# Optimization experiments

Measured on AMD Instinct MI355X. Metric: run time of the kernel, lower is better.

Reference implementation:

```python
import jax, jax.numpy as jnp
import numpy as np

THRESHOLD = 0.3
STRENGTH = 0.1
MIN_S = 0.0
MAX_S = 0.5
EPS_COS = 1e-8
EPS_LN = 1e-5

B, T, D = 1024, 64, 256
P = 2048
H = 512


def _layernorm(x, g, b):
    mu = x.mean(-1, keepdims=True)
    var = ((x - mu) ** 2).mean(-1, keepdims=True)
    return (x - mu) * jax.lax.rsqrt(var + EPS_LN) * g + b


def setup_inputs() -> dict:
    key = jax.random.key(0)
    ks = jax.random.split(key, 10)
    s = lambda fan_in: 1.0 / np.sqrt(fan_in)
    return {
        "current_feat": jax.random.normal(ks[0], (B, T, D), jnp.float32),
        "prototype": jax.random.normal(ks[1], (P, T, D), jnp.float32),
        "dd_w1": jax.random.normal(ks[2], (2 * D, H), jnp.float32) * s(2 * D),
        "dd_b1": jnp.zeros((H,), jnp.float32),
        "dd_g1": jnp.ones((H,), jnp.float32),
        "dd_be1": jnp.zeros((H,), jnp.float32),
        "dd_w2": jax.random.normal(ks[3], (H, H // 2), jnp.float32) * s(H),
        "dd_b2": jnp.zeros((H // 2,), jnp.float32),
        "dd_w3": jax.random.normal(ks[4], (H // 2, 1), jnp.float32) * s(H // 2),
        "dd_b3": jnp.zeros((1,), jnp.float32),
        "cal_w1": jax.random.normal(ks[5], (D, H), jnp.float32) * s(D),
        "cal_b1": jnp.zeros((H,), jnp.float32),
        "cal_g1": jnp.ones((H,), jnp.float32),
        "cal_be1": jnp.zeros((H,), jnp.float32),
        "cal_w2": jax.random.normal(ks[6], (H, H), jnp.float32) * s(H),
        "cal_b2": jnp.zeros((H,), jnp.float32),
        "cal_w3": jax.random.normal(ks[7], (H, D), jnp.float32) * s(H),
        "cal_b3": jnp.zeros((D,), jnp.float32),
    }


def reference(current_feat, prototype,
              dd_w1, dd_b1, dd_g1, dd_be1, dd_w2, dd_b2, dd_w3, dd_b3,
              cal_w1, cal_b1, cal_g1, cal_be1, cal_w2, cal_b2, cal_w3, cal_b3):
    # --- drift detection ---
    feat_flat = current_feat.mean(axis=1)          # [B, D]
    proto_centers = prototype.mean(axis=1)         # [P, D]
    fn = jnp.maximum(jnp.linalg.norm(feat_flat, axis=-1), EPS_COS)   # [B]
    pn = jnp.maximum(jnp.linalg.norm(proto_centers, axis=-1), EPS_COS)  # [P]
    sim = jnp.einsum('bd,pd->bp', feat_flat, proto_centers) / (fn[:, None] * pn[None, :])
    drift_score = 1.0 - sim                        # [B, P]
    is_drifted = drift_score.mean(axis=0) > THRESHOLD  # [P] bool

    # --- calibration (batched over all P, then masked scatter) ---
    global_mean = feat_flat.mean(axis=0)           # [D]
    concat = jnp.concatenate(
        [proto_centers, jnp.broadcast_to(global_mean, (proto_centers.shape[0], global_mean.shape[0]))], axis=-1)  # [P, 2D]
    h = jax.nn.relu(_layernorm(concat @ dd_w1 + dd_b1, dd_g1, dd_be1))
    h = jax.nn.relu(h @ dd_w2 + dd_b2)
    drift_conf = jax.nn.sigmoid(h @ dd_w3 + dd_b3)[:, 0]  # [P]

    c = jax.nn.relu(_layernorm(proto_centers @ cal_w1 + cal_b1, cal_g1, cal_be1))
    c = jax.nn.relu(c @ cal_w2 + cal_b2)
    delta = c @ cal_w3 + cal_b3                    # [P, D]

    strength = jnp.clip(STRENGTH * drift_conf, MIN_S, MAX_S)  # [P]
    new_center = proto_centers + strength[:, None] * delta    # [P, D]

    calibrated = jnp.where(is_drifted[:, None, None], new_center[:, None, :], prototype)  # [P, T, D]
    return calibrated, drift_score, is_drifted
```

## Files before the change

### kernel.cpp

```cpp
#include <hip/hip_runtime.h>
#include <hip/hip_bf16.h>
#include <math.h>

#define BB 1024
#define TT 64
#define DD 256
#define PP 2048
#define HH 512

typedef __attribute__((ext_vector_type(8))) short short8;
typedef __attribute__((ext_vector_type(4))) float f32x4;

__device__ __forceinline__ float blk_reduce(float v, float* sm) {
    int tid = threadIdx.x;
    #pragma unroll
    for (int o = 32; o > 0; o >>= 1) v += __shfl_down(v, o, 64);
    if ((tid & 63) == 0) sm[tid >> 6] = v;
    __syncthreads();
    float r = sm[0] + sm[1] + sm[2] + sm[3];
    __syncthreads();
    return r;
}

__global__ void reduce_bt(const float* __restrict__ x, float* __restrict__ cent,
                          __hip_bfloat16* __restrict__ centb, float* __restrict__ nrm) {
    __shared__ float sm[4];
    int r = blockIdx.x, d = threadIdx.x;
    const float* p = x + (size_t)r * TT * DD + d;
    float s = 0.f;
    #pragma unroll
    for (int t = 0; t < TT; ++t) s += p[t * DD];
    float m = s * (1.f / TT);
    cent[(size_t)r * DD + d] = m;
    centb[(size_t)r * DD + d] = __float2bfloat16(m);
    float tot = blk_reduce(m * m, sm);
    if (d == 0) nrm[r] = fmaxf(sqrtf(tot), 1e-8f);
}

__global__ void gmean_k(const float* __restrict__ ff, float* __restrict__ gmean) {
    int d = threadIdx.x;
    int b0 = blockIdx.x * 32;
    float s = 0.f;
    for (int b = b0; b < b0 + 32; ++b) s += ff[(size_t)b * DD + d];
    atomicAdd(&gmean[d], s * (1.f / BB));
}

__global__ void addvec_k(const float* __restrict__ gmean, const float* __restrict__ w1,
                         const float* __restrict__ b1, float* __restrict__ av) {
    int j = (blockIdx.x & 1) * 256 + threadIdx.x;
    int k0 = (blockIdx.x >> 1) * 64;
    float s = 0.f;
    for (int k = k0; k < k0 + 64; ++k) s += gmean[k] * w1[(size_t)(DD + k) * HH + j];
    if (k0 == 0) s += b1[j];
    atomicAdd(&av[j], s);
}

__global__ void cvt_all(const float* __restrict__ dd_w1, const float* __restrict__ dd_w2,
                        const float* __restrict__ cal_w1, const float* __restrict__ cal_w2,
                        const float* __restrict__ cal_w3,
                        __hip_bfloat16* __restrict__ t1, __hip_bfloat16* __restrict__ t2,
                        __hip_bfloat16* __restrict__ t3, __hip_bfloat16* __restrict__ t4,
                        __hip_bfloat16* __restrict__ t5) {
    int b = blockIdx.x, tid = threadIdx.x;
    const float* src; __hip_bfloat16* dst; int K, N, base;
    if (b < 512)       { src = dd_w1;  dst = t1; K = 256; N = 512; base = 0; }
    else if (b < 1024) { src = dd_w2;  dst = t2; K = 512; N = 256; base = 512; }
    else if (b < 1536) { src = cal_w1; dst = t3; K = 256; N = 512; base = 1024; }
    else if (b < 2560) { src = cal_w2; dst = t4; K = 512; N = 512; base = 1536; }
    else               { src = cal_w3; dst = t5; K = 512; N = 256; base = 2560; }
    int idx = (b - base) * 256 + tid;
    int n = idx & (N - 1);
    int k = idx >> ((N == 512) ? 9 : 8);
    dst[(size_t)n * K + k] = __float2bfloat16(src[(size_t)k * N + n]);
}

__global__ void sim_mfma(const __hip_bfloat16* __restrict__ A,
                         const __hip_bfloat16* __restrict__ Bt,
                         const float* __restrict__ fn, const float* __restrict__ pn,
                         float* __restrict__ drift, float* __restrict__ colsum) {
    int wid = ((blockIdx.x << 8) + threadIdx.x) >> 6;
    int lane = threadIdx.x & 63;
    int mw = wid >> 6, nw = wid & 63;
    int m0 = mw << 5, n0 = nw << 5;
    int lr = lane & 15, quad = lane >> 4;
    const __hip_bfloat16* pa0 = A + (size_t)(m0 + lr) * DD + quad * 8;
    const __hip_bfloat16* pa1 = pa0 + 16 * DD;
    const __hip_bfloat16* pb0 = Bt + (size_t)(n0 + lr) * DD + quad * 8;
    const __hip_bfloat16* pb1 = pb0 + 16 * DD;
    f32x4 acc00 = {0,0,0,0}, acc01 = {0,0,0,0}, acc10 = {0,0,0,0}, acc11 = {0,0,0,0};
    #pragma unroll
    for (int k = 0; k < DD; k += 32) {
        short8 a0 = *(const short8*)(pa0 + k);
        short8 a1 = *(const short8*)(pa1 + k);
        short8 b0 = *(const short8*)(pb0 + k);
        short8 b1 = *(const short8*)(pb1 + k);
        acc00 = __builtin_amdgcn_mfma_f32_16x16x32_bf16(a0, b0, acc00, 0, 0, 0);
        acc01 = __builtin_amdgcn_mfma_f32_16x16x32_bf16(a0, b1, acc01, 0, 0, 0);
        acc10 = __builtin_amdgcn_mfma_f32_16x16x32_bf16(a1, b0, acc10, 0, 0, 0);
        acc11 = __builtin_amdgcn_mfma_f32_16x16x32_bf16(a1, b1, acc11, 0, 0, 0);
    }
    int col0 = n0 + lr, col1 = col0 + 16;
    float ip0 = 1.f / pn[col0], ip1 = 1.f / pn[col1];
    float cs0 = 0.f, cs1 = 0.f;
    #pragma unroll
    for (int r = 0; r < 4; ++r) {
        int row0 = m0 + quad * 4 + r;
        int row1 = row0 + 16;
        float if0 = 1.f / fn[row0];
        float if1 = 1.f / fn[row1];
        float d00 = 1.f - acc00[r] * if0 * ip0;
        float d01 = 1.f - acc01[r] * if0 * ip1;
        float d10 = 1.f - acc10[r] * if1 * ip0;
        float d11 = 1.f - acc11[r] * if1 * ip1;
        drift[(size_t)row0 * PP + col0] = d00;
        drift[(size_t)row0 * PP + col1] = d01;
        drift[(size_t)row1 * PP + col0] = d10;
        drift[(size_t)row1 * PP + col1] = d11;
        cs0 += d00 + d10;
        cs1 += d01 + d11;
    }
    cs0 += __shfl_xor(cs0, 16, 64); cs0 += __shfl_xor(cs0, 32, 64);
    cs1 += __shfl_xor(cs1, 16, 64); cs1 += __shfl_xor(cs1, 32, 64);
    if (quad == 0) {
        atomicAdd(&colsum[col0], cs0);
        atomicAdd(&colsum[col1], cs1);
    }
}

template <int K, int OUT_BF16, int RELU>
__global__ void gemm_mfma(const __hip_bfloat16* __restrict__ A,
                          const __hip_bfloat16* __restrict__ Bt,
                          const float* __restrict__ bias,
                          void* __restrict__ Cout, int N) {
    int wid = ((blockIdx.x << 8) + threadIdx.x) >> 6;
    int lane = threadIdx.x & 63;
    int nt = N >> 5;
    int mw = wid / nt, nw = wid - mw * nt;
    int m0 = mw << 5, n0 = nw << 5;
    int lr = lane & 15, quad = lane >> 4;
    const __hip_bfloat16* pa0 = A + (size_t)(m0 + lr) * K + quad * 8;
    const __hip_bfloat16* pa1 = pa0 + 16 * K;
    const __hip_bfloat16* pb0 = Bt + (size_t)(n0 + lr) * K + quad * 8;
    const __hip_bfloat16* pb1 = pb0 + 16 * K;
    f32x4 acc00 = {0,0,0,0}, acc01 = {0,0,0,0}, acc10 = {0,0,0,0}, acc11 = {0,0,0,0};
    #pragma unroll
    for (int k = 0; k < K; k += 32) {
        short8 a0 = *(const short8*)(pa0 + k);
        short8 a1 = *(const short8*)(pa1 + k);
        short8 b0 = *(const short8*)(pb0 + k);
        short8 b1 = *(const short8*)(pb1 + k);
        acc00 = __builtin_amdgcn_mfma_f32_16x16x32_bf16(a0, b0, acc00, 0, 0, 0);
        acc01 = __builtin_amdgcn_mfma_f32_16x16x32_bf16(a0, b1, acc01, 0, 0, 0);
        acc10 = __builtin_amdgcn_mfma_f32_16x16x32_bf16(a1, b0, acc10, 0, 0, 0);
        acc11 = __builtin_amdgcn_mfma_f32_16x16x32_bf16(a1, b1, acc11, 0, 0, 0);
    }
    int col0 = n0 + lr, col1 = col0 + 16;
    float bi0 = bias[col0], bi1 = bias[col1];
    #pragma unroll
    for (int r = 0; r < 4; ++r) {
        int row0 = m0 + quad * 4 + r;
        int row1 = row0 + 16;
        float v00 = acc00[r] + bi0, v01 = acc01[r] + bi1;
        float v10 = acc10[r] + bi0, v11 = acc11[r] + bi1;
        if (RELU) {
            v00 = fmaxf(v00, 0.f); v01 = fmaxf(v01, 0.f);
            v10 = fmaxf(v10, 0.f); v11 = fmaxf(v11, 0.f);
        }
        if (OUT_BF16) {
            __hip_bfloat16* C = (__hip_bfloat16*)Cout;
            C[(size_t)row0 * N + col0] = __float2bfloat16(v00);
            C[(size_t)row0 * N + col1] = __float2bfloat16(v01);
            C[(size_t)row1 * N + col0] = __float2bfloat16(v10);
            C[(size_t)row1 * N + col1] = __float2bfloat16(v11);
        } else {
            float* C = (float*)Cout;
            C[(size_t)row0 * N + col0] = v00;
            C[(size_t)row0 * N + col1] = v01;
            C[(size_t)row1 * N + col0] = v10;
            C[(size_t)row1 * N + col1] = v11;
        }
    }
}

__global__ void ln_relu(const float* __restrict__ X, __hip_bfloat16* __restrict__ Y,
                        const float* __restrict__ g, const float* __restrict__ be) {
    __shared__ float sm[4];
    int r = blockIdx.x, tid = threadIdx.x;
    const float* row = X + (size_t)r * HH;
    float x0 = row[tid], x1 = row[tid + 256];
    float mu = blk_reduce(x0 + x1, sm) * (1.f / HH);
    float d0 = x0 - mu, d1 = x1 - mu;
    float var = blk_reduce(d0 * d0 + d1 * d1, sm) * (1.f / HH);
    float rs = rsqrtf(var + 1e-5f);
    float y0 = fmaxf(d0 * rs * g[tid] + be[tid], 0.f);
    float y1 = fmaxf(d1 * rs * g[tid + 256] + be[tid + 256], 0.f);
    __hip_bfloat16* yrow = Y + (size_t)r * HH;
    yrow[tid] = __float2bfloat16(y0);
    yrow[tid + 256] = __float2bfloat16(y1);
}

__global__ void conf_k(const __hip_bfloat16* __restrict__ h2, const float* __restrict__ w3,
                       const float* __restrict__ b3, const float* __restrict__ colsum,
                       float* __restrict__ strength, float* __restrict__ out_is) {
    __shared__ float sm[4];
    int p = blockIdx.x, tid = threadIdx.x;
    float v = __bfloat162float(h2[(size_t)p * 256 + tid]) * w3[tid];
    float s = blk_reduce(v, sm);
    if (tid == 0) {
        float conf = 1.f / (1.f + expf(-(s + b3[0])));
        float st = fminf(fmaxf(0.1f * conf, 0.f), 0.5f);
        strength[p] = st;
        out_is[p] = (colsum[p] * (1.f / BB) > 0.3f) ? 1.f : 0.f;
    }
}

__global__ void finalize_k(const float* __restrict__ pc, const float* __restrict__ delta,
                           const float* __restrict__ strength, const float* __restrict__ colsum,
                           const float* __restrict__ proto, float* __restrict__ out) {
    int p = blockIdx.x, d = threadIdx.x;
    bool dr = colsum[p] * (1.f / BB) > 0.3f;
    float* o = out + (size_t)p * TT * DD + d;
    if (dr) {
        float nc = pc[(size_t)p * DD + d] + strength[p] * delta[(size_t)p * DD + d];
        #pragma unroll 4
        for (int t = 0; t < TT; ++t) o[t * DD] = nc;
    } else {
        const float* pr = proto + (size_t)p * TT * DD + d;
        #pragma unroll 4
        for (int t = 0; t < TT; ++t) o[t * DD] = pr[t * DD];
    }
}

extern "C" void kernel_launch(void* const* d_in, const int* in_sizes, int n_in,
                              void* d_out, int out_size, void* d_ws, size_t ws_size,
                              hipStream_t stream) {
    const float* cf     = (const float*)d_in[0];
    const float* proto  = (const float*)d_in[1];
    const float* dd_w1  = (const float*)d_in[2];
    const float* dd_b1  = (const float*)d_in[3];
    const float* dd_g1  = (const float*)d_in[4];
    const float* dd_be1 = (const float*)d_in[5];
    const float* dd_w2  = (const float*)d_in[6];
    const float* dd_b2  = (const float*)d_in[7];
    const float* dd_w3  = (const float*)d_in[8];
    const float* dd_b3  = (const float*)d_in[9];
    const float* cal_w1 = (const float*)d_in[10];
    const float* cal_b1 = (const float*)d_in[11];
    const float* cal_g1 = (const float*)d_in[12];
    const float* cal_be1= (const float*)d_in[13];
    const float* cal_w2 = (const float*)d_in[14];
    const float* cal_b2 = (const float*)d_in[15];
    const float* cal_w3 = (const float*)d_in[16];
    const float* cal_b3 = (const float*)d_in[17];

    float* out_cal   = (float*)d_out;
    float* out_drift = out_cal + (size_t)PP * TT * DD;
    float* out_is    = out_drift + (size_t)BB * PP;

    float* w = (float*)d_ws;
    float* gmean    = w;
    float* colsum   = w + 256;
    float* addvec   = w + 2304;
    float* fn       = w + 2816;
    float* pn       = w + 3840;
    float* strength = w + 5888;
    float* ff       = w + 8192;
    float* pc       = w + 270336;
    float* buf1     = w + 794624;
    float* delta    = w + 1843200;
    __hip_bfloat16* ffb     = (__hip_bfloat16*)(w + 2367488);
    __hip_bfloat16* pcb     = ffb + 262144;
    __hip_bfloat16* w1t_dd  = pcb + 524288;
    __hip_bfloat16* w2t_dd  = w1t_dd + 131072;
    __hip_bfloat16* w1t_cal = w2t_dd + 131072;
    __hip_bfloat16* w2t_cal = w1t_cal + 131072;
    __hip_bfloat16* w3t_cal = w2t_cal + 262144;
    __hip_bfloat16* act1b   = w3t_cal + 131072;
    __hip_bfloat16* act3b   = act1b + 1048576;
    __hip_bfloat16* act2b   = act3b + 1048576;

    hipMemsetAsync(d_ws, 0, 2816 * sizeof(float), stream);

    reduce_bt<<<BB, 256, 0, stream>>>(cf, ff, ffb, fn);
    reduce_bt<<<PP, 256, 0, stream>>>(proto, pc, pcb, pn);
    gmean_k<<<32, 256, 0, stream>>>(ff, gmean);
    addvec_k<<<8, 256, 0, stream>>>(gmean, dd_w1, dd_b1, addvec);
    cvt_all<<<3072, 256, 0, stream>>>(dd_w1, dd_w2, cal_w1, cal_w2, cal_w3,
                                      w1t_dd, w2t_dd, w1t_cal, w2t_cal, w3t_cal);

    sim_mfma<<<512, 256, 0, stream>>>(ffb, pcb, fn, pn, out_drift, colsum);

    gemm_mfma<256, 0, 0><<<256, 256, 0, stream>>>(pcb, w1t_dd, addvec, buf1, HH);
    ln_relu<<<PP, 256, 0, stream>>>(buf1, act1b, dd_g1, dd_be1);
    gemm_mfma<512, 1, 1><<<128, 256, 0, stream>>>(act1b, w2t_dd, dd_b2, act2b, 256);
    conf_k<<<PP, 256, 0, stream>>>(act2b, dd_w3, dd_b3, colsum, strength, out_is);

    gemm_mfma<256, 0, 0><<<256, 256, 0, stream>>>(pcb, w1t_cal, cal_b1, buf1, HH);
    ln_relu<<<PP, 256, 0, stream>>>(buf1, act1b, cal_g1, cal_be1);
    gemm_mfma<512, 1, 1><<<256, 256, 0, stream>>>(act1b, w2t_cal, cal_b2, act3b, HH);
    gemm_mfma<512, 0, 0><<<128, 256, 0, stream>>>(act3b, w3t_cal, cal_b3, delta, 256);

    finalize_k<<<PP, 256, 0, stream>>>(pc, delta, strength, colsum, proto, out_cal);
}
```

Before: 418.1 us.

## Fuse prep, sim/addvec, dual MLP branches, and vectorize finalize

Merges the row reductions, global mean and weight transposes into one prep kernel. It also folds the addvec GEMV into the similarity kernel, and runs both first-layer GEMMs as one concatenated GEMM with a dual LayerNorm kernel. The second-layer GEMMs and the GEMM3/confidence stages are co-scheduled in shared launches. The finalize copy is vectorized to float4 with more threads per time step. The aim is to cut launch overhead and serialization between small kernels, and to improve bandwidth in the dominant copy, at the cost of larger, more branchy kernels.

```diff
diff --git a/kernel.cpp b/kernel.cpp
--- a/kernel.cpp
+++ b/kernel.cpp
@@ -22,63 +22,85 @@
     return r;
 }
 
-__global__ void reduce_bt(const float* __restrict__ x, float* __restrict__ cent,
-                          __hip_bfloat16* __restrict__ centb, float* __restrict__ nrm) {
+__global__ void prep_k(const float* __restrict__ cf, const float* __restrict__ proto,
+                       const float* __restrict__ dd_w1, const float* __restrict__ dd_w2,
+                       const float* __restrict__ cal_w1, const float* __restrict__ cal_w2,
+                       const float* __restrict__ cal_w3,
+                       float* __restrict__ gmean8, float* __restrict__ fn,
+                       float* __restrict__ pn, float* __restrict__ pc,
+                       __hip_bfloat16* __restrict__ ffb, __hip_bfloat16* __restrict__ pcb,
+                       __hip_bfloat16* __restrict__ w1cat, __hip_bfloat16* __restrict__ w2dd,
+                       __hip_bfloat16* __restrict__ w2cal, __hip_bfloat16* __restrict__ w3cal) {
     __shared__ float sm[4];
-    int r = blockIdx.x, d = threadIdx.x;
-    const float* p = x + (size_t)r * TT * DD + d;
-    float s = 0.f;
-    #pragma unroll
-    for (int t = 0; t < TT; ++t) s += p[t * DD];
-    float m = s * (1.f / TT);
-    cent[(size_t)r * DD + d] = m;
-    centb[(size_t)r * DD + d] = __float2bfloat16(m);
-    float tot = blk_reduce(m * m, sm);
-    if (d == 0) nrm[r] = fmaxf(sqrtf(tot), 1e-8f);
-}
-
-__global__ void gmean_k(const float* __restrict__ ff, float* __restrict__ gmean) {
-    int d = threadIdx.x;
-    int b0 = blockIdx.x * 32;
-    float s = 0.f;
-    for (int b = b0; b < b0 + 32; ++b) s += ff[(size_t)b * DD + d];
-    atomicAdd(&gmean[d], s * (1.f / BB));
-}
-
-__global__ void addvec_k(const float* __restrict__ gmean, const float* __restrict__ w1,
-                         const float* __restrict__ b1, float* __restrict__ av) {
-    int j = (blockIdx.x & 1) * 256 + threadIdx.x;
-    int k0 = (blockIdx.x >> 1) * 64;
-    float s = 0.f;
-    for (int k = k0; k < k0 + 64; ++k) s += gmean[k] * w1[(size_t)(DD + k) * HH + j];
-    if (k0 == 0) s += b1[j];
-    atomicAdd(&av[j], s);
-}
-
-__global__ void cvt_all(const float* __restrict__ dd_w1, const float* __restrict__ dd_w2,
-                        const float* __restrict__ cal_w1, const float* __restrict__ cal_w2,
-                        const float* __restrict__ cal_w3,
-                        __hip_bfloat16* __restrict__ t1, __hip_bfloat16* __restrict__ t2,
-                        __hip_bfloat16* __restrict__ t3, __hip_bfloat16* __restrict__ t4,
-                        __hip_bfloat16* __restrict__ t5) {
     int b = blockIdx.x, tid = threadIdx.x;
-    const float* src; __hip_bfloat16* dst; int K, N, base;
-    if (b < 512)       { src = dd_w1;  dst = t1; K = 256; N = 512; base = 0; }
-    else if (b < 1024) { src = dd_w2;  dst = t2; K = 512; N = 256; base = 512; }
-    else if (b < 1536) { src = cal_w1; dst = t3; K = 256; N = 512; base = 1024; }
-    else if (b < 2560) { src = cal_w2; dst = t4; K = 512; N = 512; base = 1536; }
-    else               { src = cal_w3; dst = t5; K = 512; N = 256; base = 2560; }
-    int idx = (b - base) * 256 + tid;
-    int n = idx & (N - 1);
-    int k = idx >> ((N == 512) ? 9 : 8);
-    dst[(size_t)n * K + k] = __float2bfloat16(src[(size_t)k * N + n]);
-}
-
-__global__ void sim_mfma(const __hip_bfloat16* __restrict__ A,
-                         const __hip_bfloat16* __restrict__ Bt,
-                         const float* __restrict__ fn, const float* __restrict__ pn,
-                         float* __restrict__ drift, float* __restrict__ colsum) {
-    int wid = ((blockIdx.x << 8) + threadIdx.x) >> 6;
+    if (b < 1024) {
+        const float* p = cf + (size_t)b * TT * DD + tid;
+        float s = 0.f;
+        #pragma unroll
+        for (int t = 0; t < TT; ++t) s += p[t * DD];
+        float m = s * (1.f / TT);
+        ffb[(size_t)b * DD + tid] = __float2bfloat16(m);
+        atomicAdd(&gmean8[(b & 7) * 256 + tid], m * (1.f / BB));
+        float tot = blk_reduce(m * m, sm);
+        if (tid == 0) fn[b] = fmaxf(sqrtf(tot), 1e-8f);
+    } else if (b < 3072) {
+        int r = b - 1024;
+        const float* p = proto + (size_t)r * TT * DD + tid;
+        float s = 0.f;
+        #pragma unroll
+        for (int t = 0; t < TT; ++t) s += p[t * DD];
+        float m = s * (1.f / TT);
+        pc[(size_t)r * DD + tid] = m;
+        pcb[(size_t)r * DD + tid] = __float2bfloat16(m);
+        float tot = blk_reduce(m * m, sm);
+        if (tid == 0) pn[r] = fmaxf(sqrtf(tot), 1e-8f);
+    } else {
+        int idx = (b - 3072) * 256 + tid;
+        if (idx < 262144) {
+            int half = idx >> 17;
+            int i = idx & 131071;
+            int n = i & 511, k = i >> 9;
+            const float* src = half ? cal_w1 : dd_w1;
+            w1cat[(size_t)(half * 512 + n) * 256 + k] = __float2bfloat16(src[(size_t)k * 512 + n]);
+        } else if (idx < 393216) {
+            int i = idx - 262144;
+            int n = i & 255, k = i >> 8;
+            w2dd[(size_t)n * 512 + k] = __float2bfloat16(dd_w2[(size_t)k * 256 + n]);
+        } else if (idx < 655360) {
+            int i = idx - 393216;
+            int n = i & 511, k = i >> 9;
+            w2cal[(size_t)n * 512 + k] = __float2bfloat16(cal_w2[(size_t)k * 512 + n]);
+        } else {
+            int i = idx - 655360;
+            int n = i & 255, k = i >> 8;
+            w3cal[(size_t)n * 512 + k] = __float2bfloat16(cal_w3[(size_t)k * 256 + n]);
+        }
+    }
+}
+
+__global__ void sim_addvec_k(const __hip_bfloat16* __restrict__ A,
+                             const __hip_bfloat16* __restrict__ Bt,
+                             const float* __restrict__ fn, const float* __restrict__ pn,
+                             const float* __restrict__ gmean8,
+                             const float* __restrict__ dd_w1, const float* __restrict__ dd_b1,
+                             float* __restrict__ drift, float* __restrict__ colsum,
+                             float* __restrict__ addvec) {
+    if (blockIdx.x >= 512) {
+        __shared__ float gmk[256];
+        int tid = threadIdx.x;
+        float g = 0.f;
+        #pragma unroll
+        for (int s = 0; s < 8; ++s) g += gmean8[s * 256 + tid];
+        gmk[tid] = g;
+        __syncthreads();
+        int j = (blockIdx.x - 512) * 256 + tid;
+        float s = dd_b1[j];
+        #pragma unroll 8
+        for (int k = 0; k < 256; ++k) s = fmaf(gmk[k], dd_w1[(size_t)(256 + k) * 512 + j], s);
+        addvec[j] = s;
+        return;
+    }
+    int wid = (blockIdx.x << 2) + (threadIdx.x >> 6);
     int lane = threadIdx.x & 63;
     int mw = wid >> 6, nw = wid & 63;
     int m0 = mw << 5, n0 = nw << 5;
@@ -128,14 +150,13 @@
 }
 
 template <int K, int OUT_BF16, int RELU>
-__global__ void gemm_mfma(const __hip_bfloat16* __restrict__ A,
-                          const __hip_bfloat16* __restrict__ Bt,
-                          const float* __restrict__ bias,
-                          void* __restrict__ Cout, int N) {
-    int wid = ((blockIdx.x << 8) + threadIdx.x) >> 6;
-    int lane = threadIdx.x & 63;
-    int nt = N >> 5;
-    int mw = wid / nt, nw = wid - mw * nt;
+__device__ __forceinline__ void gemm_tile(const __hip_bfloat16* __restrict__ A,
+                                          const __hip_bfloat16* __restrict__ Bt,
+                                          const float* __restrict__ bias0,
+                                          const float* __restrict__ bias1, int split,
+                                          void* __restrict__ Cout, int N, int lognt,
+                                          int wid, int lane) {
+    int mw = wid >> lognt, nw = wid & ((1 << lognt) - 1);
     int m0 = mw << 5, n0 = nw << 5;
     int lr = lane & 15, quad = lane >> 4;
     const __hip_bfloat16* pa0 = A + (size_t)(m0 + lr) * K + quad * 8;
@@ -155,7 +176,8 @@
         acc11 = __builtin_amdgcn_mfma_f32_16x16x32_bf16(a1, b1, acc11, 0, 0, 0);
     }
     int col0 = n0 + lr, col1 = col0 + 16;
-    float bi0 = bias[col0], bi1 = bias[col1];
+    float bi0 = (col0 < split) ? bias0[col0] : bias1[col0 - split];
+    float bi1 = (col1 < split) ? bias0[col1] : bias1[col1 - split];
     #pragma unroll
     for (int r = 0; r < 4; ++r) {
         int row0 = m0 + quad * 4 + r;
@@ -182,34 +204,81 @@
     }
 }
 
-__global__ void ln_relu(const float* __restrict__ X, __hip_bfloat16* __restrict__ Y,
-                        const float* __restrict__ g, const float* __restrict__ be) {
+__global__ void gemm1_k(const __hip_bfloat16* __restrict__ pcb,
+                        const __hip_bfloat16* __restrict__ w1cat,
+                        const float* __restrict__ addvec, const float* __restrict__ cal_b1,
+                        float* __restrict__ buf1) {
+    int wid = (blockIdx.x << 2) + (threadIdx.x >> 6);
+    gemm_tile<256, 0, 0>(pcb, w1cat, addvec, cal_b1, 512, buf1, 1024, 5,
+                         wid, threadIdx.x & 63);
+}
+
+__global__ void ln2_k(const float* __restrict__ X,
+                      __hip_bfloat16* __restrict__ Ydd, __hip_bfloat16* __restrict__ Ycal,
+                      const float* __restrict__ gdd, const float* __restrict__ bedd,
+                      const float* __restrict__ gcal, const float* __restrict__ becal) {
     __shared__ float sm[4];
     int r = blockIdx.x, tid = threadIdx.x;
-    const float* row = X + (size_t)r * HH;
-    float x0 = row[tid], x1 = row[tid + 256];
-    float mu = blk_reduce(x0 + x1, sm) * (1.f / HH);
-    float d0 = x0 - mu, d1 = x1 - mu;
-    float var = blk_reduce(d0 * d0 + d1 * d1, sm) * (1.f / HH);
-    float rs = rsqrtf(var + 1e-5f);
-    float y0 = fmaxf(d0 * rs * g[tid] + be[tid], 0.f);
-    float y1 = fmaxf(d1 * rs * g[tid + 256] + be[tid + 256], 0.f);
-    __hip_bfloat16* yrow = Y + (size_t)r * HH;
-    yrow[tid] = __float2bfloat16(y0);
-    yrow[tid + 256] = __float2bfloat16(y1);
-}
-
-__global__ void conf_k(const __hip_bfloat16* __restrict__ h2, const float* __restrict__ w3,
-                       const float* __restrict__ b3, const float* __restrict__ colsum,
-                       float* __restrict__ strength, float* __restrict__ out_is) {
+    const float* row = X + (size_t)r * 1024;
+    {
+        float x0 = row[tid], x1 = row[tid + 256];
+        float mu = blk_reduce(x0 + x1, sm) * (1.f / HH);
+        float d0 = x0 - mu, d1 = x1 - mu;
+        float var = blk_reduce(d0 * d0 + d1 * d1, sm) * (1.f / HH);
+        float rs = rsqrtf(var + 1e-5f);
+        __hip_bfloat16* y = Ydd + (size_t)r * HH;
+        y[tid]       = __float2bfloat16(fmaxf(d0 * rs * gdd[tid] + bedd[tid], 0.f));
+        y[tid + 256] = __float2bfloat16(fmaxf(d1 * rs * gdd[tid + 256] + bedd[tid + 256], 0.f));
+    }
+    {
+        float x0 = row[512 + tid], x1 = row[768 + tid];
+        float mu = blk_reduce(x0 + x1, sm) * (1.f / HH);
+        float d0 = x0 - mu, d1 = x1 - mu;
+        float var = blk_reduce(d0 * d0 + d1 * d1, sm) * (1.f / HH);
+        float rs = rsqrtf(var + 1e-5f);
+        __hip_bfloat16* y = Ycal + (size_t)r * HH;
+        y[tid]       = __float2bfloat16(fmaxf(d0 * rs * gcal[tid] + becal[tid], 0.f));
+        y[tid + 256] = __float2bfloat16(fmaxf(d1 * rs * gcal[tid + 256] + becal[tid + 256], 0.f));
+    }
+}
+
+__global__ void gemm2_k(const __hip_bfloat16* __restrict__ act_dd,
+                        const __hip_bfloat16* __restrict__ act_cal,
+                        const __hip_bfloat16* __restrict__ w2dd,
+                        const __hip_bfloat16* __restrict__ w2cal,
+                        const float* __restrict__ dd_b2, const float* __restrict__ cal_b2,
+                        __hip_bfloat16* __restrict__ act2b, __hip_bfloat16* __restrict__ act3b) {
+    int lane = threadIdx.x & 63;
+    if (blockIdx.x < 128) {
+        int wid = (blockIdx.x << 2) + (threadIdx.x >> 6);
+        gemm_tile<512, 1, 1>(act_dd, w2dd, dd_b2, dd_b2, 1 << 30, act2b, 256, 3, wid, lane);
+    } else {
+        int wid = ((blockIdx.x - 128) << 2) + (threadIdx.x >> 6);
+        gemm_tile<512, 1, 1>(act_cal, w2cal, cal_b2, cal_b2, 1 << 30, act3b, 512, 4, wid, lane);
+    }
+}
+
+__global__ void gemm3_conf_k(const __hip_bfloat16* __restrict__ act3b,
+                             const __hip_bfloat16* __restrict__ w3cal,
+                             const float* __restrict__ cal_b3,
+                             const __hip_bfloat16* __restrict__ act2b,
+                             const float* __restrict__ dd_w3, const float* __restrict__ dd_b3,
+                             const float* __restrict__ colsum,
+                             float* __restrict__ delta, float* __restrict__ strength,
+                             float* __restrict__ out_is) {
+    if (blockIdx.x < 128) {
+        int wid = (blockIdx.x << 2) + (threadIdx.x >> 6);
+        gemm_tile<512, 0, 0>(act3b, w3cal, cal_b3, cal_b3, 1 << 30, delta, 256, 3,
+                             wid, threadIdx.x & 63);
+        return;
+    }
     __shared__ float sm[4];
-    int p = blockIdx.x, tid = threadIdx.x;
-    float v = __bfloat162float(h2[(size_t)p * 256 + tid]) * w3[tid];
+    int p = blockIdx.x - 128, tid = threadIdx.x;
+    float v = __bfloat162float(act2b[(size_t)p * 256 + tid]) * dd_w3[tid];
     float s = blk_reduce(v, sm);
     if (tid == 0) {
-        float conf = 1.f / (1.f + expf(-(s + b3[0])));
-        float st = fminf(fmaxf(0.1f * conf, 0.f), 0.5f);
-        strength[p] = st;
+        float conf = 1.f / (1.f + expf(-(s + dd_b3[0])));
+        strength[p] = fminf(fmaxf(0.1f * conf, 0.f), 0.5f);
         out_is[p] = (colsum[p] * (1.f / BB) > 0.3f) ? 1.f : 0.f;
     }
 }
@@ -217,17 +286,25 @@
 __global__ void finalize_k(const float* __restrict__ pc, const float* __restrict__ delta,
                            const float* __restrict__ strength, const float* __restrict__ colsum,
                            const float* __restrict__ proto, float* __restrict__ out) {
-    int p = blockIdx.x, d = threadIdx.x;
+    int p = blockIdx.x;
+    int d4 = (threadIdx.x & 63) << 2;
+    int t0 = threadIdx.x >> 6;
     bool dr = colsum[p] * (1.f / BB) > 0.3f;
-    float* o = out + (size_t)p * TT * DD + d;
+    float* o = out + (size_t)p * TT * DD;
     if (dr) {
-        float nc = pc[(size_t)p * DD + d] + strength[p] * delta[(size_t)p * DD + d];
-        #pragma unroll 4
-        for (int t = 0; t < TT; ++t) o[t * DD] = nc;
+        float s = strength[p];
+        float4 pcv = *(const float4*)(pc + (size_t)p * DD + d4);
+        float4 dv  = *(const float4*)(delta + (size_t)p * DD + d4);
+        float4 nc = make_float4(fmaf(s, dv.x, pcv.x), fmaf(s, dv.y, pcv.y),
+                                fmaf(s, dv.z, pcv.z), fmaf(s, dv.w, pcv.w));
+        #pragma unroll
+        for (int t = t0; t < TT; t += 4)
+            *(float4*)(o + t * DD + d4) = nc;
     } else {
-        const float* pr = proto + (size_t)p * TT * DD + d;
-        #pragma unroll 4
-        for (int t = 0; t < TT; ++t) o[t * DD] = pr[t * DD];
+        const float* pr = proto + (size_t)p * TT * DD;
+        #pragma unroll
+        for (int t = t0; t < TT; t += 4)
+            *(float4*)(o + t * DD + d4) = *(const float4*)(pr + t * DD + d4);
     }
 }
 
@@ -258,47 +335,39 @@
     float* out_is    = out_drift + (size_t)BB * PP;
 
     float* w = (float*)d_ws;
-    float* gmean    = w;
-    float* colsum   = w + 256;
-    float* addvec   = w + 2304;
-    float* fn       = w + 2816;
-    float* pn       = w + 3840;
-    float* strength = w + 5888;
-    float* ff       = w + 8192;
-    float* pc       = w + 270336;
-    float* buf1     = w + 794624;
-    float* delta    = w + 1843200;
-    __hip_bfloat16* ffb     = (__hip_bfloat16*)(w + 2367488);
-    __hip_bfloat16* pcb     = ffb + 262144;
-    __hip_bfloat16* w1t_dd  = pcb + 524288;
-    __hip_bfloat16* w2t_dd  = w1t_dd + 131072;
-    __hip_bfloat16* w1t_cal = w2t_dd + 131072;
-    __hip_bfloat16* w2t_cal = w1t_cal + 131072;
-    __hip_bfloat16* w3t_cal = w2t_cal + 262144;
-    __hip_bfloat16* act1b   = w3t_cal + 131072;
-    __hip_bfloat16* act3b   = act1b + 1048576;
-    __hip_bfloat16* act2b   = act3b + 1048576;
-
-    hipMemsetAsync(d_ws, 0, 2816 * sizeof(float), stream);
-
-    reduce_bt<<<BB, 256, 0, stream>>>(cf, ff, ffb, fn);
-    reduce_bt<<<PP, 256, 0, stream>>>(proto, pc, pcb, pn);
-    gmean_k<<<32, 256, 0, stream>>>(ff, gmean);
-    addvec_k<<<8, 256, 0, stream>>>(gmean, dd_w1, dd_b1, addvec);
-    cvt_all<<<3072, 256, 0, stream>>>(dd_w1, dd_w2, cal_w1, cal_w2, cal_w3,
-                                      w1t_dd, w2t_dd, w1t_cal, w2t_cal, w3t_cal);
-
-    sim_mfma<<<512, 256, 0, stream>>>(ffb, pcb, fn, pn, out_drift, colsum);
-
-    gemm_mfma<256, 0, 0><<<256, 256, 0, stream>>>(pcb, w1t_dd, addvec, buf1, HH);
-    ln_relu<<<PP, 256, 0, stream>>>(buf1, act1b, dd_g1, dd_be1);
-    gemm_mfma<512, 1, 1><<<128, 256, 0, stream>>>(act1b, w2t_dd, dd_b2, act2b, 256);
-    conf_k<<<PP, 256, 0, stream>>>(act2b, dd_w3, dd_b3, colsum, strength, out_is);
-
-    gemm_mfma<256, 0, 0><<<256, 256, 0, stream>>>(pcb, w1t_cal, cal_b1, buf1, HH);
-    ln_relu<<<PP, 256, 0, stream>>>(buf1, act1b, cal_g1, cal_be1);
-    gemm_mfma<512, 1, 1><<<256, 256, 0, stream>>>(act1b, w2t_cal, cal_b2, act3b, HH);
-    gemm_mfma<512, 0, 0><<<128, 256, 0, stream>>>(act3b, w3t_cal, cal_b3, delta, 256);
-
+    float* gmean8   = w;
+    float* colsum   = w + 2048;
+    float* addvec   = w + 4096;
+    float* fn       = w + 4608;
+    float* pn       = w + 5632;
+    float* strength = w + 7680;
+    float* pc       = w + 9728;
+    float* buf1     = w + 534016;
+    float* delta    = w + 2631168;
+    __hip_bfloat16* bb = (__hip_bfloat16*)(w + 3155456);
+    __hip_bfloat16* ffb     = bb;
+    __hip_bfloat16* pcb     = bb + 262144;
+    __hip_bfloat16* w1cat   = bb + 786432;
+    __hip_bfloat16* w2dd    = bb + 1048576;
+    __hip_bfloat16* w2cal   = bb + 1179648;
+    __hip_bfloat16* w3cal   = bb + 1441792;
+    __hip_bfloat16* act_dd  = bb + 1572864;
+    __hip_bfloat16* act_cal = bb + 2621440;
+    __hip_bfloat16* act2b   = bb + 3670016;
+    __hip_bfloat16* act3b   = bb + 4194304;
+
+    hipMemsetAsync(d_ws, 0, 4096 * sizeof(float), stream);
+
+    prep_k<<<6144, 256, 0, stream>>>(cf, proto, dd_w1, dd_w2, cal_w1, cal_w2, cal_w3,
+                                     gmean8, fn, pn, pc, ffb, pcb,
+                                     w1cat, w2dd, w2cal, w3cal);
+    sim_addvec_k<<<514, 256, 0, stream>>>(ffb, pcb, fn, pn, gmean8, dd_w1, dd_b1,
+                                          out_drift, colsum, addvec);
+    gemm1_k<<<512, 256, 0, stream>>>(pcb, w1cat, addvec, cal_b1, buf1);
+    ln2_k<<<PP, 256, 0, stream>>>(buf1, act_dd, act_cal, dd_g1, dd_be1, cal_g1, cal_be1);
+    gemm2_k<<<384, 256, 0, stream>>>(act_dd, act_cal, w2dd, w2cal, dd_b2, cal_b2,
+                                     act2b, act3b);
+    gemm3_conf_k<<<2176, 256, 0, stream>>>(act3b, w3cal, cal_b3, act2b, dd_w3, dd_b3,
+                                           colsum, delta, strength, out_is);
     finalize_k<<<PP, 256, 0, stream>>>(pc, delta, strength, colsum, proto, out_cal);
 }
```

After: 417.9 us. Within noise of the previous version (-0.1%).
